# Performance work log

Hardware: AMD Instinct MI355X
Metric: run time of the kernel (lower is better)

The kernel has to match this reference:

```python
import jax, jax.numpy as jnp
import numpy as np

B, S, H, EMB, VOCAB, LABEL, NUM_LAYERS = 32, 512, 256, 256, 32000, 16, 3


def _before(x):  # shift right along seq dim, zero-pad front
    z = jnp.zeros_like(x[:, :1])
    return jnp.concatenate([z, x[:, :-1]], axis=1)


def _after(x):  # shift left along seq dim, zero-pad end
    z = jnp.zeros_like(x[:, :1])
    return jnp.concatenate([x[:, 1:], z], axis=1)


def setup_inputs() -> dict:
    key = jax.random.key(0)
    ks = jax.random.split(key, 12)
    p = lambda k, shape: (0.02 * jax.random.normal(k, shape)).astype(jnp.float32)
    return {
        "span_nodes": jnp.zeros((1,), jnp.int32),
        "bert_vec": jnp.zeros((1,), jnp.float32),
        "node_text": jax.random.randint(ks[0], (B, S), 0, VOCAB),
        "word_mask": jnp.ones((B, S), jnp.float32),
        "sent_mask": jnp.ones((1,), jnp.int32),
        "node_feature": jnp.zeros((1,), jnp.float32),
        "adj": jnp.zeros((1,), jnp.int32),
        # embedding + emb_proj
        "E": p(ks[1], (VOCAB, EMB)),
        "Wp": p(ks[2], (EMB, H)), "bp": jnp.zeros((H,), jnp.float32),
        # SCell: W(3H->7H, no bias), U(emb->7H, no bias), V(H->7H, bias)
        "Ws": p(ks[3], (3 * H, 7 * H)), "Us": p(ks[4], (EMB, 7 * H)),
        "Vs": p(ks[5], (H, 7 * H)), "bVs": jnp.zeros((7 * H,), jnp.float32),
        # GCell: W(H->2H, no bias), w(H->H, no bias), U(H->2H, bias), u(H->H, bias)
        "WgW": p(ks[6], (H, 2 * H)), "Wgw": p(ks[7], (H, H)),
        "UgU": p(ks[8], (H, 2 * H)), "bgU": jnp.zeros((2 * H,), jnp.float32),
        "ugu": p(ks[9], (H, H)), "bgu": jnp.zeros((H,), jnp.float32),
        # output head
        "Wo": p(ks[10], (H, LABEL)), "bo": jnp.zeros((LABEL,), jnp.float32),
    }


def _slstm(node_text, word_mask, E, Wp, bp, Ws, Us, Vs, bVs,
           WgW, Wgw, UgU, bgU, ugu, bgu, Wo, bo):
    mask = word_mask[..., None]                      # [B,S,1]
    emb = E[node_text]                               # [B,S,EMB]
    proj = (emb @ Wp + bp) * mask                    # [B,S,H] (dropout=identity in eval)
    h = proj
    c = proj
    g = h.mean(1)                                    # [B,H]
    c_g = c.mean(1)                                  # [B,H]
    xU = emb @ Us                                    # [B,S,7H] hoisted (constant per layer)
    neg = ((1.0 - word_mask) * 1e16)[..., None]      # [B,S,1]
    for _ in range(NUM_LAYERS):
        h = h * mask
        c = c * mask
        # SCell
        hcat = jnp.concatenate([_before(h), h, _after(h)], axis=-1)   # [B,S,3H]
        gates = hcat @ Ws + xU + (g @ Vs + bVs)[:, None, :]           # [B,S,7H]
        gi, gl, gr, gf, gs, go, gu = jnp.split(gates, 7, axis=-1)
        gu = jnp.tanh(gu)
        # sigmoid then softmax over the stacked-gate dim (note: o stays raw, as in source)
        stk = jax.nn.softmax(jax.nn.sigmoid(jnp.stack([gi, gl, gr, gf, gs], axis=-2)), axis=-2)
        gi, gl, gr, gf, gs = (stk[..., k, :] for k in range(5))
        new_c = _before(c) * gl + c * gf + gr * _after(c) + gs * c_g[:, None, :] + gi * gu
        new_h = go * jnp.tanh(new_c)
        # GCell (uses pre-update h, c)
        h_avg = h.mean(1)                                             # [B,H]
        fo = jax.nn.sigmoid(g @ WgW + h_avg @ UgU + bgU)              # [B,2H]
        f_g, o_g = jnp.split(fo, 2, axis=-1)
        f_w = jax.nn.sigmoid((g @ Wgw)[:, None, :] + h @ ugu + bgu) - neg   # [B,S,H]
        f_w = jax.nn.softmax(f_w, axis=1)
        new_c_g = f_g * c_g + (c * f_w).sum(1)
        new_g = o_g * jnp.tanh(new_c_g)
        h, c, g, c_g = new_h, new_c, new_g, new_c_g
    return (g @ Wo + bo, g.mean(0) @ Wo + bo)


def reference(span_nodes, bert_vec, node_text, word_mask, sent_mask, node_feature, adj,
              E, Wp, bp, Ws, Us, Vs, bVs, WgW, Wgw, UgU, bgU, ugu, bgu, Wo, bo):
    return _slstm(node_text, word_mask, E, Wp, bp, Ws, Us, Vs, bVs,
                  WgW, Wgw, UgU, bgU, ugu, bgu, Wo, bo)
```

## Files before the change

kernel.cpp:

```cpp
#include <hip/hip_runtime.h>
#include <math.h>

#define B_      32
#define S_      512
#define H_      256
#define EMB_    256
#define M_      (B_*S_)
#define N7_     1792
#define NG_     2048
#define NS_     2560
#define KA_     1024
#define LABEL_  16

#define BM 256
#define BN 256
#define BK 64
#define NT (KA_/BK)
#define EBM 64

typedef __bf16 bf16x8 __attribute__((ext_vector_type(8)));
typedef float  f32x4  __attribute__((ext_vector_type(4)));
typedef unsigned short us8 __attribute__((ext_vector_type(8)));

__device__ __forceinline__ float sigf(float x){ return 1.f/(1.f+__expf(-x)); }

__device__ __forceinline__ unsigned short f2bf(float f){
    union { float f; unsigned int u; } v; v.f = f;
    unsigned int r = v.u + 0x7FFFu + ((v.u >> 16) & 1u);
    return (unsigned short)(r >> 16);
}
__device__ __forceinline__ float bf2f(unsigned short u){
    union { unsigned int i; float f; } v; v.i = ((unsigned int)u) << 16; return v.f;
}

#define WAUG_TH (NG_*KA_/8)
#define WPT_TH  (H_*EMB_/8)
#define EMB_TH  (M_*EMB_/8)
#define PREP_TH (WAUG_TH + WPT_TH + EMB_TH)

__global__ void prep_all(const float* __restrict__ Ws, const float* __restrict__ Us,
                         const float* __restrict__ ugu, const float* __restrict__ Wp,
                         const int* __restrict__ idx, const float* __restrict__ E,
                         unsigned short* __restrict__ WaugT, unsigned short* __restrict__ WpT,
                         unsigned short* __restrict__ embbf, unsigned short* __restrict__ zpage){
    long u = (long)blockIdx.x*256 + threadIdx.x;
    if(u < 512) zpage[u] = 0;
    if(u < WAUG_TH){
        int j  = (int)(u >> 7);
        int kc = ((int)u & 127) * 8;
        int tg = j >> 7, rem = j & 127, p = rem >> 4, t = tg*16 + (rem & 15);
        us8 o;
        if(p < 7){
            int col = p*256 + t;
            #pragma unroll
            for(int x=0;x<8;x++){
                int k = kc + x;
                float v = (k < 768) ? Ws[(long)k*N7_ + col] : Us[(long)(k-768)*N7_ + col];
                o[x] = f2bf(v);
            }
        } else {
            #pragma unroll
            for(int x=0;x<8;x++){
                int k = kc + x;
                float v = (k >= 256 && k < 512) ? ugu[(k-256)*H_ + t] : 0.f;
                o[x] = f2bf(v);
            }
        }
        *(us8*)&WaugT[(long)j*KA_ + kc] = o;
    } else if(u < WAUG_TH + WPT_TH){
        long v = u - WAUG_TH;
        int j = (int)(v >> 5), kc = ((int)v & 31)*8;
        us8 o;
        #pragma unroll
        for(int x=0;x<8;x++) o[x] = f2bf(Wp[(long)(kc+x)*H_ + j]);
        *(us8*)&WpT[(long)j*EMB_ + kc] = o;
    } else if(u < PREP_TH){
        long v = u - WAUG_TH - WPT_TH;
        int i = (int)(v >> 5), kc = ((int)v & 31)*8;
        const float* src = E + (size_t)idx[i]*EMB_ + kc;
        us8 o;
        #pragma unroll
        for(int x=0;x<8;x++) o[x] = f2bf(src[x]);
        *(us8*)&embbf[(size_t)i*EMB_ + kc] = o;
    }
}

__global__ __launch_bounds__(256, 2) void embed_mfma(
        const unsigned short* __restrict__ embbf, const unsigned short* __restrict__ WpT,
        const float* __restrict__ bp, const float* __restrict__ mask,
        unsigned short* __restrict__ h0b, float* __restrict__ c0){
    __shared__ unsigned short As[2][EBM*32];
    __shared__ unsigned short Bs[2][H_*32];
    int tid = threadIdx.x, w = tid>>6, l = tid&63, fr = l&15, fq = l>>4;
    int m0 = blockIdx.x * EBM;
    f32x4 acc[4][4];
    #pragma unroll
    for(int m=0;m<4;m++)
        #pragma unroll
        for(int n=0;n<4;n++) acc[m][n] = (f32x4){0.f,0.f,0.f,0.f};

    auto stage = [&](int buf, int kt){
        {
            int row = tid >> 2;
            int k0 = ((tid & 3) ^ ((row >> 1) & 3)) * 8;
            const unsigned short* src = embbf + (size_t)(m0+row)*EMB_ + kt + k0;
            __builtin_amdgcn_global_load_lds(
                (const __attribute__((address_space(1))) unsigned int*)src,
                (__attribute__((address_space(3))) unsigned int*)(&As[buf][w*512]),
                16, 0, 0);
        }
        #pragma unroll
        for(int q=0;q<4;q++){
            int v = q*256 + tid;
            int col = v >> 2;
            int k0 = ((v & 3) ^ ((col >> 1) & 3)) * 8;
            const unsigned short* src = WpT + (size_t)col*EMB_ + kt + k0;
            __builtin_amdgcn_global_load_lds(
                (const __attribute__((address_space(1))) unsigned int*)src,
                (__attribute__((address_space(3))) unsigned int*)(&Bs[buf][(q*256 + w*64)*8]),
                16, 0, 0);
        }
    };

    stage(0, 0);
    __syncthreads();
    int cur = 0;
    for(int step=0; step<EMB_/32; step++){
        if(step+1 < EMB_/32) stage(cur^1, (step+1)*32);
        bf16x8 bfv[4];
        #pragma unroll
        for(int n=0;n<4;n++){
            int colr = w*64 + n*16 + fr;
            int slot = fq ^ ((colr >> 1) & 3);
            bfv[n] = *(const bf16x8*)(&Bs[cur][colr*32 + slot*8]);
        }
        #pragma unroll
        for(int m=0;m<4;m++){
            int rowr = m*16 + fr;
            int slot = fq ^ ((rowr >> 1) & 3);
            bf16x8 af = *(const bf16x8*)(&As[cur][rowr*32 + slot*8]);
            #pragma unroll
            for(int n=0;n<4;n++)
                acc[m][n] = __builtin_amdgcn_mfma_f32_16x16x32_bf16(af, bfv[n], acc[m][n], 0,0,0);
        }
        __syncthreads();
        cur ^= 1;
    }
    #pragma unroll
    for(int m=0;m<4;m++){
        #pragma unroll
        for(int j=0;j<4;j++){
            int i = m0 + m*16 + fq*4 + j;
            float mk = mask[i];
            #pragma unroll
            for(int n=0;n<4;n++){
                int col = w*64 + n*16 + fr;
                float v = (acc[m][n][j] + bp[col]) * mk;
                h0b[(size_t)i*H_ + col] = f2bf(v);
                c0 [(size_t)i*H_ + col] = v;
            }
        }
    }
}

__global__ void reduce_mean_s(const unsigned short* __restrict__ h, float* __restrict__ outA,
                              float* __restrict__ outB){
    __shared__ float part[4][256];
    int b = blockIdx.x;
    int hh = threadIdx.x & 255, sg = threadIdx.x >> 8;
    float s = 0.f;
    long base = ((long)b*S_ + sg*128)*H_ + hh;
    for(int ss=0; ss<128; ss++) s += bf2f(h[base + (long)ss*H_]);
    part[sg][hh] = s;
    __syncthreads();
    if(threadIdx.x < 256){
        float t = (part[0][hh]+part[1][hh]+part[2][hh]+part[3][hh]) * (1.f/S_);
        outA[b*H_+hh] = t;
        if(outB) outB[b*H_+hh] = t;
    }
}

__global__ void small_gemm(const float* __restrict__ g, const float* __restrict__ havg,
                           const float* __restrict__ Vs, const float* __restrict__ bVs,
                           const float* __restrict__ Wgw, const float* __restrict__ bgu,
                           const float* __restrict__ WgW, const float* __restrict__ UgU,
                           const float* __restrict__ bgU, float* __restrict__ smalls){
    __shared__ float gs[256], hs[256];
    int b = blockIdx.y, t0 = threadIdx.x;
    gs[t0] = g[b*H_+t0];
    hs[t0] = havg[b*H_+t0];
    __syncthreads();
    int j = blockIdx.x*256 + t0;
    float acc;
    if(j < NG_){
        int tg = j >> 7, rem = j & 127, p = rem >> 4, t = tg*16 + (rem & 15);
        if(p < 7){
            int col = p*256 + t;
            acc = bVs[col];
            for(int k=0;k<H_;k++) acc += gs[k]*Vs[k*N7_+col];
        } else {
            acc = bgu[t];
            for(int k=0;k<H_;k++) acc += gs[k]*Wgw[k*H_+t];
        }
    } else {
        int jj = j - NG_;
        acc = bgU[jj];
        for(int k=0;k<H_;k++) acc += gs[k]*WgW[k*512+jj] + hs[k]*UgU[k*512+jj];
        acc = sigf(acc);
    }
    smalls[b*NS_+j] = acc;
}

__global__ __launch_bounds__(512, 2) void layer_mfma(
        const unsigned short* __restrict__ hbf, const unsigned short* __restrict__ embbf,
        const unsigned short* __restrict__ WaugT, const unsigned short* __restrict__ zpage,
        const float* __restrict__ c_old, const float* __restrict__ cg_old,
        const float* __restrict__ smalls, const float* __restrict__ mask,
        unsigned short* __restrict__ hbf_new, float* __restrict__ c_new,
        float* __restrict__ lpart, float* __restrict__ apart, float* __restrict__ hpart){
    __shared__ unsigned short As[2][BM*BK];
    __shared__ unsigned short Bs[2][BN*BK];
    __shared__ float red[8][16][3];
    int tid = threadIdx.x;
    int w = tid >> 6, l = tid & 63;
    int fr = l & 15, fq = l >> 4;
    int wr = w >> 1, wcl = w & 1;
    int m0 = blockIdx.x * BM;
    int n0 = blockIdx.y * BN;
    int b  = m0 >> 9;

    f32x4 acc[4][8];
    #pragma unroll
    for(int m=0;m<4;m++)
        #pragma unroll
        for(int n=0;n<8;n++) acc[m][n] = (f32x4){0.f,0.f,0.f,0.f};

    int rowc[2][2], k0a[2][2];
    #pragma unroll
    for(int p=0;p<2;p++)
        #pragma unroll
        for(int q=0;q<2;q++){
            int u = q*512 + tid;
            int row = p*128 + (u>>3);
            rowc[p][q] = row;
            k0a[p][q]  = ((u & 7) ^ (row & 7)) * 8;
        }
    const unsigned short* srcA[2][2];
    const unsigned short* srcB[2][2];
    #pragma unroll
    for(int hf=0;hf<2;hf++)
        #pragma unroll
        for(int q=0;q<2;q++){
            int u = q*512 + tid;
            int col = hf*128 + (u>>3);
            int k0 = ((u & 7) ^ (col & 7)) * 8;
            srcB[hf][q] = WaugT + (size_t)(n0 + col)*KA_ + k0;
        }
    auto setupA = [&](int r){
        #pragma unroll
        for(int p=0;p<2;p++)
            #pragma unroll
            for(int q=0;q<2;q++){
                int i = m0 + rowc[p][q];
                if(r < 3){
                    int si = (i & (S_-1)) + r - 1;
                    srcA[p][q] = ((unsigned)si < (unsigned)S_)
                               ? hbf + (size_t)(i + r - 1)*H_ + k0a[p][q]
                               : zpage + k0a[p][q];
                } else {
                    srcA[p][q] = embbf + (size_t)i*EMB_ + k0a[p][q];
                }
            }
    };
    auto advance = [&](){
        #pragma unroll
        for(int p=0;p<2;p++)
            #pragma unroll
            for(int q=0;q<2;q++){ srcA[p][q] += BK; srcB[p][q] += BK; }
    };
    auto stage_half = [&](int buf, int ph){
        if(ph < 2){
            #pragma unroll
            for(int q=0;q<2;q++)
                __builtin_amdgcn_global_load_lds(
                    (const __attribute__((address_space(1))) unsigned int*)srcA[ph][q],
                    (__attribute__((address_space(3))) unsigned int*)
                        (&As[buf][ph*8192 + (q*512 + w*64)*8]),
                    16, 0, 0);
        } else {
            int hf = ph - 2;
            #pragma unroll
            for(int q=0;q<2;q++)
                __builtin_amdgcn_global_load_lds(
                    (const __attribute__((address_space(1))) unsigned int*)srcB[hf][q],
                    (__attribute__((address_space(3))) unsigned int*)
                        (&Bs[buf][hf*8192 + (q*512 + w*64)*8]),
                    16, 0, 0);
        }
    };

    setupA(0);
    stage_half(0, 0); stage_half(0, 1); stage_half(0, 2); stage_half(0, 3);
    advance();

    bf16x8 afv[4];
    #pragma unroll 1
    for(int t=0; t<NT; ++t){
        int buf = t & 1;
        int st  = t + 1;
        if(st < NT){
            if((st & 3) == 0) setupA(st >> 2);
            stage_half(buf^1, 0);
            asm volatile("s_waitcnt vmcnt(2)" ::: "memory");
        } else {
            asm volatile("s_waitcnt vmcnt(0)" ::: "memory");
        }
        __builtin_amdgcn_s_barrier();
        #pragma unroll
        for(int p=0;p<4;p++){
            int ks = p >> 1, nh = p & 1;
            if(nh == 0){
                #pragma unroll
                for(int m=0;m<4;m++){
                    int row  = wr*64 + m*16 + fr;
                    int slot = (ks*4 + fq) ^ (row & 7);
                    afv[m] = *(const bf16x8*)(&As[buf][row*BK + slot*8]);
                }
            }
            bf16x8 bfv[4];
            #pragma unroll
            for(int nn=0;nn<4;nn++){
                int col  = wcl*128 + (nh*4+nn)*16 + fr;
                int slot = (ks*4 + fq) ^ (col & 7);
                bfv[nn] = *(const bf16x8*)(&Bs[buf][col*BK + slot*8]);
            }
            if(p < 3 && st < NT) stage_half(buf^1, p+1);
            __builtin_amdgcn_s_barrier();
            asm volatile("s_waitcnt lgkmcnt(0)" ::: "memory");
            __builtin_amdgcn_sched_barrier(0);
            __builtin_amdgcn_s_setprio(1);
            #pragma unroll
            for(int m=0;m<4;m++)
                #pragma unroll
                for(int nn=0;nn<4;nn++)
                    acc[m][nh*4+nn] = __builtin_amdgcn_mfma_f32_16x16x32_bf16(
                                          afv[m], bfv[nn], acc[m][nh*4+nn], 0,0,0);
            __builtin_amdgcn_s_setprio(0);
            __builtin_amdgcn_s_barrier();
        }
        if(st < NT) advance();
    }

    int t = (n0 >> 3) + wcl*16 + fr;
    float sm[8];
    #pragma unroll
    for(int n=0;n<8;n++) sm[n] = smalls[b*NS_ + n0 + wcl*128 + n*16 + fr];
    float cgv = cg_old[b*H_ + t];
    float lsum = 0.f, asum = 0.f, hsum = 0.f;
    #pragma unroll
    for(int m=0;m<4;m++){
        #pragma unroll
        for(int j=0;j<4;j++){
            int i = m0 + wr*64 + m*16 + fq*4 + j;
            int s = i & (S_-1);
            float gv[8];
            #pragma unroll
            for(int n=0;n<8;n++) gv[n] = acc[m][n][j] + sm[n];
            float ei=__expf(sigf(gv[0])), el=__expf(sigf(gv[1])), er=__expf(sigf(gv[2]));
            float ef=__expf(sigf(gv[3])), es=__expf(sigf(gv[4]));
            float inv = 1.f/(ei+el+er+ef+es);
            float c0v = c_old[(size_t)i*H_ + t];
            float cbv = (s>0)      ? c_old[(size_t)(i-1)*H_ + t] : 0.f;
            float cav = (s<S_-1)   ? c_old[(size_t)(i+1)*H_ + t] : 0.f;
            float tu = tanhf(gv[6]);
            float nc = (cbv*el + c0v*ef + er*cav + es*cgv + ei*tu)*inv;
            float nh2 = gv[5]*tanhf(nc);
            float mk = mask[i];
            float ncm = nc*mk, nhm = nh2*mk;
            c_new [(size_t)i*H_ + t] = ncm;
            hbf_new[(size_t)i*H_ + t] = f2bf(nhm);
            float e = __expf(sigf(gv[7]) - (1.f - mk)*1e16f);
            lsum += e;
            asum += e*c0v;
            hsum += nhm;
        }
    }
    #pragma unroll
    for(int off=16; off<64; off<<=1){
        lsum += __shfl_xor(lsum, off);
        asum += __shfl_xor(asum, off);
        hsum += __shfl_xor(hsum, off);
    }
    if(l < 16){ red[w][l][0]=lsum; red[w][l][1]=asum; red[w][l][2]=hsum; }
    __syncthreads();
    if(tid < 32){
        int wc2 = tid >> 4, fr2 = tid & 15;
        float L = 0.f, A = 0.f, Hh = 0.f;
        #pragma unroll
        for(int k=0;k<4;k++){
            L  += red[2*k + wc2][fr2][0];
            A  += red[2*k + wc2][fr2][1];
            Hh += red[2*k + wc2][fr2][2];
        }
        int tt = (n0 >> 3) + wc2*16 + fr2;
        int by = blockIdx.x;
        lpart[by*H_ + tt] = L;
        apart[by*H_ + tt] = A;
        hpart[by*H_ + tt] = Hh;
    }
}

__global__ void gcell2x(const float* __restrict__ lpart, const float* __restrict__ apart,
                        const float* __restrict__ hpart, const float* __restrict__ cg_old,
                        const float* __restrict__ smalls,
                        float* __restrict__ g_new, float* __restrict__ cg_new,
                        float* __restrict__ havg_out){
    int b = blockIdx.x, t = threadIdx.x;
    float L = 0.f, A = 0.f, Hs = 0.f;
    for(int ci=0; ci<2; ci++){
        int by = b*2 + ci;
        L  += lpart[by*H_ + t];
        A  += apart[by*H_ + t];
        Hs += hpart[by*H_ + t];
    }
    float fg = smalls[b*NS_ + NG_ + t];
    float og = smalls[b*NS_ + NG_ + 256 + t];
    float ncg = fg*cg_old[b*H_+t] + A/L;
    g_new[b*H_+t]    = og*tanhf(ncg);
    cg_new[b*H_+t]   = ncg;
    havg_out[b*H_+t] = Hs * (1.f/S_);
}

__global__ void outk(const float* __restrict__ g, const float* __restrict__ Wo,
                     const float* __restrict__ bo, float* __restrict__ out){
    __shared__ float o1[B_*LABEL_];
    int t = threadIdx.x;
    if(t < B_*LABEL_){
        int b = t/LABEL_, j = t%LABEL_;
        float acc = bo[j];
        for(int k=0;k<H_;k++) acc += g[b*H_+k]*Wo[k*LABEL_+j];
        o1[t] = acc;
        out[t] = acc;
    }
    __syncthreads();
    if(t < LABEL_){
        float s = 0.f;
        for(int b=0;b<B_;b++) s += o1[b*LABEL_+t];
        out[B_*LABEL_+t] = s*(1.f/B_);
    }
}

extern "C" void kernel_launch(void* const* d_in, const int* in_sizes, int n_in,
                              void* d_out, int out_size, void* d_ws, size_t ws_size,
                              hipStream_t stream){
    const int*   node_text = (const int*)  d_in[2];
    const float* word_mask = (const float*)d_in[3];
    const float* E   = (const float*)d_in[7];
    const float* Wp  = (const float*)d_in[8];
    const float* bp  = (const float*)d_in[9];
    const float* Ws  = (const float*)d_in[10];
    const float* Us  = (const float*)d_in[11];
    const float* Vs  = (const float*)d_in[12];
    const float* bVs = (const float*)d_in[13];
    const float* WgW = (const float*)d_in[14];
    const float* Wgw = (const float*)d_in[15];
    const float* UgU = (const float*)d_in[16];
    const float* bgU = (const float*)d_in[17];
    const float* ugu = (const float*)d_in[18];
    const float* bgu = (const float*)d_in[19];
    const float* Wo  = (const float*)d_in[20];
    const float* bo  = (const float*)d_in[21];

    float* w = (float*)d_ws;
    size_t off = 0;
    auto alloc = [&](size_t nfloats){ float* p = w + off; off += nfloats; return p; };
    unsigned short* WaugT = (unsigned short*)alloc((size_t)NG_*KA_/2);
    unsigned short* zpage = (unsigned short*)alloc(256);
    unsigned short* WpT   = (unsigned short*)alloc((size_t)H_*EMB_/2);
    unsigned short* embbf = (unsigned short*)alloc((size_t)M_*EMB_/2);
    unsigned short* hbf[2] = { (unsigned short*)alloc((size_t)M_*H_/2),
                               (unsigned short*)alloc((size_t)M_*H_/2) };
    float* cb[2]  = { alloc((size_t)M_*H_), alloc((size_t)M_*H_) };
    float* lpart  = alloc((size_t)(M_/BM)*H_);
    float* apart  = alloc((size_t)(M_/BM)*H_);
    float* hpart  = alloc((size_t)(M_/BM)*H_);
    float* gb[2]  = { alloc(B_*H_), alloc(B_*H_) };
    float* cgb[2] = { alloc(B_*H_), alloc(B_*H_) };
    float* havg   = alloc(B_*H_);
    float* smalls = alloc((size_t)B_*NS_);

    prep_all<<<(PREP_TH + 255)/256, 256, 0, stream>>>(Ws, Us, ugu, Wp, node_text, E,
                                                      WaugT, WpT, embbf, zpage);
    embed_mfma<<<M_/EBM, 256, 0, stream>>>(embbf, WpT, bp, word_mask, hbf[0], cb[0]);
    reduce_mean_s<<<B_, 1024, 0, stream>>>(hbf[0], gb[0], cgb[0]);

    int cur = 0;
    for(int layer=0; layer<3; layer++){
        int nxt = cur ^ 1;
        const float* havg_in = (layer == 0) ? gb[0] : havg;
        small_gemm<<<dim3(NS_/256, B_), 256, 0, stream>>>(gb[cur], havg_in, Vs, bVs,
                                                          Wgw, bgu, WgW, UgU, bgU, smalls);
        layer_mfma<<<dim3(M_/BM, NG_/BN), 512, 0, stream>>>(hbf[cur], embbf, WaugT, zpage,
                                                            cb[cur], cgb[cur], smalls, word_mask,
                                                            hbf[nxt], cb[nxt],
                                                            lpart, apart, hpart);
        gcell2x<<<B_, 256, 0, stream>>>(lpart, apart, hpart, cgb[cur], smalls,
                                        gb[nxt], cgb[nxt], havg);
        cur = nxt;
    }
    outk<<<1, 512, 0, stream>>>(gb[cur], Wo, bo, (float*)d_out);
}
```

Baseline: 383.5 us.

## Fuse initial mean into embed epilogue and restructure layer GEMM staging

The embed GEMM now produces per-block column partial sums of the projected state, and a small gcell0 kernel reduces them, replacing the separate reduce_mean_s pass that re-read the whole bf16 h buffer. In layer_mfma, the staging of the next K tile is moved entirely inside the four-phase inner loop with a single vmcnt(0) wait at phase 0, and a sched_barrier is added after the MFMA block. The small_gemm loops are also unrolled by four. The mean now sums fp32 values rather than bf16-rounded ones, and the full vmcnt(0) wait may expose more global-load latency than the old partial wait.

```diff
diff --git a/kernel.cpp b/kernel.cpp
--- a/kernel.cpp
+++ b/kernel.cpp
@@ -88,7 +88,8 @@
 __global__ __launch_bounds__(256, 2) void embed_mfma(
         const unsigned short* __restrict__ embbf, const unsigned short* __restrict__ WpT,
         const float* __restrict__ bp, const float* __restrict__ mask,
-        unsigned short* __restrict__ h0b, float* __restrict__ c0){
+        unsigned short* __restrict__ h0b, float* __restrict__ c0,
+        float* __restrict__ epart){
     __shared__ unsigned short As[2][EBM*32];
     __shared__ unsigned short Bs[2][H_*32];
     int tid = threadIdx.x, w = tid>>6, l = tid&63, fr = l&15, fq = l>>4;
@@ -146,6 +147,7 @@
         __syncthreads();
         cur ^= 1;
     }
+    float hsum[4] = {0.f, 0.f, 0.f, 0.f};
     #pragma unroll
     for(int m=0;m<4;m++){
         #pragma unroll
@@ -158,26 +160,31 @@
                 float v = (acc[m][n][j] + bp[col]) * mk;
                 h0b[(size_t)i*H_ + col] = f2bf(v);
                 c0 [(size_t)i*H_ + col] = v;
-            }
-        }
-    }
-}
-
-__global__ void reduce_mean_s(const unsigned short* __restrict__ h, float* __restrict__ outA,
-                              float* __restrict__ outB){
-    __shared__ float part[4][256];
-    int b = blockIdx.x;
-    int hh = threadIdx.x & 255, sg = threadIdx.x >> 8;
+                hsum[n] += v;
+            }
+        }
+    }
+    #pragma unroll
+    for(int n=0;n<4;n++){
+        hsum[n] += __shfl_xor(hsum[n], 16);
+        hsum[n] += __shfl_xor(hsum[n], 32);
+    }
+    if(l < 16){
+        #pragma unroll
+        for(int n=0;n<4;n++)
+            epart[(size_t)blockIdx.x*H_ + w*64 + n*16 + l] = hsum[n];
+    }
+}
+
+__global__ void gcell0(const float* __restrict__ epart,
+                       float* __restrict__ g0, float* __restrict__ cg0){
+    int b = blockIdx.x, t = threadIdx.x;
     float s = 0.f;
-    long base = ((long)b*S_ + sg*128)*H_ + hh;
-    for(int ss=0; ss<128; ss++) s += bf2f(h[base + (long)ss*H_]);
-    part[sg][hh] = s;
-    __syncthreads();
-    if(threadIdx.x < 256){
-        float t = (part[0][hh]+part[1][hh]+part[2][hh]+part[3][hh]) * (1.f/S_);
-        outA[b*H_+hh] = t;
-        if(outB) outB[b*H_+hh] = t;
-    }
+    #pragma unroll
+    for(int ch=0; ch<8; ch++) s += epart[(size_t)(b*8+ch)*H_ + t];
+    s *= (1.f/S_);
+    g0[b*H_+t]  = s;
+    cg0[b*H_+t] = s;
 }
 
 __global__ void small_gemm(const float* __restrict__ g, const float* __restrict__ havg,
@@ -197,14 +204,17 @@
         if(p < 7){
             int col = p*256 + t;
             acc = bVs[col];
+            #pragma unroll 4
             for(int k=0;k<H_;k++) acc += gs[k]*Vs[k*N7_+col];
         } else {
             acc = bgu[t];
+            #pragma unroll 4
             for(int k=0;k<H_;k++) acc += gs[k]*Wgw[k*H_+t];
         }
     } else {
         int jj = j - NG_;
         acc = bgU[jj];
+        #pragma unroll 4
         for(int k=0;k<H_;k++) acc += gs[k]*WgW[k*512+jj] + hs[k]*UgU[k*512+jj];
         acc = sigf(acc);
     }
@@ -308,17 +318,13 @@
     for(int t=0; t<NT; ++t){
         int buf = t & 1;
         int st  = t + 1;
-        if(st < NT){
-            if((st & 3) == 0) setupA(st >> 2);
-            stage_half(buf^1, 0);
-            asm volatile("s_waitcnt vmcnt(2)" ::: "memory");
-        } else {
-            asm volatile("s_waitcnt vmcnt(0)" ::: "memory");
-        }
-        __builtin_amdgcn_s_barrier();
         #pragma unroll
         for(int p=0;p<4;p++){
             int ks = p >> 1, nh = p & 1;
+            if(p == 0){
+                asm volatile("s_waitcnt vmcnt(0)" ::: "memory");
+                __builtin_amdgcn_s_barrier();
+            }
             if(nh == 0){
                 #pragma unroll
                 for(int m=0;m<4;m++){
@@ -334,7 +340,10 @@
                 int slot = (ks*4 + fq) ^ (col & 7);
                 bfv[nn] = *(const bf16x8*)(&Bs[buf][col*BK + slot*8]);
             }
-            if(p < 3 && st < NT) stage_half(buf^1, p+1);
+            if(st < NT){
+                if(p == 0 && (st & 3) == 0) setupA(st >> 2);
+                stage_half(buf^1, p);
+            }
             __builtin_amdgcn_s_barrier();
             asm volatile("s_waitcnt lgkmcnt(0)" ::: "memory");
             __builtin_amdgcn_sched_barrier(0);
@@ -346,6 +355,7 @@
                     acc[m][nh*4+nn] = __builtin_amdgcn_mfma_f32_16x16x32_bf16(
                                           afv[m], bfv[nn], acc[m][nh*4+nn], 0,0,0);
             __builtin_amdgcn_s_setprio(0);
+            __builtin_amdgcn_sched_barrier(0);
             __builtin_amdgcn_s_barrier();
         }
         if(st < NT) advance();
@@ -484,6 +494,7 @@
     float* lpart  = alloc((size_t)(M_/BM)*H_);
     float* apart  = alloc((size_t)(M_/BM)*H_);
     float* hpart  = alloc((size_t)(M_/BM)*H_);
+    float* epart  = alloc((size_t)(M_/EBM)*H_);
     float* gb[2]  = { alloc(B_*H_), alloc(B_*H_) };
     float* cgb[2] = { alloc(B_*H_), alloc(B_*H_) };
     float* havg   = alloc(B_*H_);
@@ -491,8 +502,9 @@
 
     prep_all<<<(PREP_TH + 255)/256, 256, 0, stream>>>(Ws, Us, ugu, Wp, node_text, E,
                                                       WaugT, WpT, embbf, zpage);
-    embed_mfma<<<M_/EBM, 256, 0, stream>>>(embbf, WpT, bp, word_mask, hbf[0], cb[0]);
-    reduce_mean_s<<<B_, 1024, 0, stream>>>(hbf[0], gb[0], cgb[0]);
+    embed_mfma<<<M_/EBM, 256, 0, stream>>>(embbf, WpT, bp, word_mask,
+                                           hbf[0], cb[0], epart);
+    gcell0<<<B_, 256, 0, stream>>>(epart, gb[0], cgb[0]);
 
     int cur = 0;
     for(int layer=0; layer<3; layer++){
```

Result: slower. 412.9 us (+7.7%).
